# Kernel tuning notes

Measured on AMD Instinct MI355X. Metric: run time of the kernel, lower is better.

## Reference

```python
import jax, jax.numpy as jnp
import numpy as np

N_NODES = 50000
N_EDGES = 800000
D_FEAT = 64
N_CLASSES = 40


def setup_inputs() -> dict:
    key = jax.random.key(0)
    ks = jax.random.split(key, 8)
    x = jax.random.normal(ks[0], (N_NODES, D_FEAT), dtype=jnp.float32)
    edge_index = jax.random.randint(ks[1], (2, N_EDGES), 0, N_NODES, dtype=jnp.int64)
    # GCNConv weights (glorot-ish scale) and post-aggregation biases
    s1 = 1.0 / np.sqrt(D_FEAT)
    W1 = jax.random.normal(ks[2], (D_FEAT, D_FEAT), dtype=jnp.float32) * s1
    b1 = jnp.zeros((D_FEAT,), dtype=jnp.float32)
    W2 = jax.random.normal(ks[3], (D_FEAT, D_FEAT), dtype=jnp.float32) * s1
    b2 = jnp.zeros((D_FEAT,), dtype=jnp.float32)
    W3 = jax.random.normal(ks[4], (D_FEAT, N_CLASSES), dtype=jnp.float32) * s1
    b3 = jnp.zeros((N_CLASSES,), dtype=jnp.float32)
    return {"x": x, "edge_index": edge_index, "W1": W1, "b1": b1,
            "W2": W2, "b2": b2, "W3": W3, "b3": b3}


def _gcn_layer(x, src, dst, norm, W, b, n_nodes):
    # dense transform then normalized neighbor aggregation (PyG GCNConv)
    h = x @ W                                   # [N, out]
    msgs = h[src] * norm[:, None]               # gather over edges [E+N, out]
    agg = jax.ops.segment_sum(msgs, dst, num_segments=n_nodes)
    return agg + b


def reference(x, edge_index, W1, b1, W2, b2, W3, b3):
    n = x.shape[0]
    loops = jnp.arange(n, dtype=edge_index.dtype)
    src = jnp.concatenate([edge_index[0], loops])   # add self-loops
    dst = jnp.concatenate([edge_index[1], loops])
    # symmetric normalization: deg over targets incl. self-loops
    deg = jax.ops.segment_sum(jnp.ones_like(dst, dtype=x.dtype), dst, num_segments=n)
    dinv = jnp.where(deg > 0, jax.lax.rsqrt(deg), 0.0)
    norm = dinv[src] * dinv[dst]                    # [E+N]
    for W, b in ((W1, b1), (W2, b2), (W3, b3)):
        x = jax.nn.relu(_gcn_layer(x, src, dst, norm, W, b, n))
        # dropout treated as identity (deterministic eval reference)
    return jax.nn.log_softmax(x, axis=-1)
```

## Files before the change

kernel.cpp:

```cpp
#include <hip/hip_runtime.h>
#include <math.h>


#define DF 64
#define TB 256
#define NPART 8

__device__ __forceinline__ unsigned short f2bf(float f) {
    union { float f; unsigned u; } c; c.f = f;
    unsigned u = c.u;
    return (unsigned short)((u + 0x7fffu + ((u >> 16) & 1u)) >> 16);
}
__device__ __forceinline__ float bf2f(unsigned short h) {
    union { unsigned u; float f; } c; c.u = ((unsigned)h) << 16;
    return c.f;
}

__global__ void zero_int_kernel(int* __restrict__ p, int n) {
    int i = blockIdx.x * blockDim.x + threadIdx.x;
    if (i < n) p[i] = 0;
}

__global__ void count_deg_part_kernel(const int* __restrict__ dst, int* __restrict__ deg,
                                      int e, int psize) {
    const int p   = blockIdx.x & (NPART - 1);
    const int sl  = blockIdx.x / NPART;
    const int nsl = gridDim.x / NPART;
    const int lo = p * psize, hi = lo + psize;
    for (int i = sl * TB + threadIdx.x; i < e; i += nsl * TB) {
        int d = dst[i];
        if (d >= lo && d < hi) atomicAdd(&deg[d], 1);
    }
}

__global__ void scan_block_kernel(const int* __restrict__ deg, int* __restrict__ ex,
                                  int* __restrict__ bsum, float* __restrict__ dinv, int n) {
    __shared__ int s[TB];
    const int t = threadIdx.x;
    const int i = blockIdx.x * TB + t;
    int v = (i < n) ? deg[i] : 0;
    if (i < n) dinv[i] = rsqrtf((float)(v + 1));
    s[t] = v; __syncthreads();
#pragma unroll
    for (int o = 1; o < TB; o <<= 1) {
        int u = (t >= o) ? s[t - o] : 0;
        __syncthreads();
        s[t] += u;
        __syncthreads();
    }
    if (i < n) ex[i] = s[t] - v;
    if (t == TB - 1) bsum[blockIdx.x] = s[TB - 1];
}

__global__ void scan_sums_kernel(int* __restrict__ bsum, int nb) {
    __shared__ int s[TB];
    const int t = threadIdx.x;
    int v = (t < nb) ? bsum[t] : 0;
    s[t] = v; __syncthreads();
#pragma unroll
    for (int o = 1; o < TB; o <<= 1) {
        int u = (t >= o) ? s[t - o] : 0;
        __syncthreads();
        s[t] += u;
        __syncthreads();
    }
    if (t < nb) bsum[t] = s[t] - v;
}

__global__ void add_offsets_kernel(int* __restrict__ ex, const int* __restrict__ bsum,
                                   int* __restrict__ cursor, int n) {
    int i = blockIdx.x * blockDim.x + threadIdx.x;
    if (i < n) {
        int r = ex[i] + bsum[blockIdx.x];
        ex[i] = r;
        cursor[i] = r;
    }
}

__global__ void fill_csr_part_kernel(const int* __restrict__ src, const int* __restrict__ dst,
                                     int* __restrict__ cursor,
                                     unsigned short* __restrict__ cidx, int e, int psize) {
    const int p   = blockIdx.x & (NPART - 1);
    const int sl  = blockIdx.x / NPART;
    const int nsl = gridDim.x / NPART;
    const int lo = p * psize, hi = lo + psize;
    for (int i = sl * TB + threadIdx.x; i < e; i += nsl * TB) {
        int d = dst[i];
        if (d >= lo && d < hi) {
            int pos = atomicAdd(&cursor[d], 1);
            cidx[pos] = (unsigned short)src[i];
        }
    }
}

template <int NC, typename TIN>
__global__ __launch_bounds__(256) void gemm_kernel(const TIN* __restrict__ X,
                                                   const float* __restrict__ W,
                                                   const float* __restrict__ dinv,
                                                   unsigned short* __restrict__ G, int M) {
    __shared__ float Ws[64 * NC];
    __shared__ float Xs[16][65];
    const int tx = threadIdx.x;
    const int ty = threadIdx.y;
    const int tid = ty * 16 + tx;
    for (int i = tid; i < 64 * NC / 4; i += 256)
        ((float4*)Ws)[i] = ((const float4*)W)[i];
    const int row0 = blockIdx.x * 16;
    {
        int r = tid / 16, c4 = tid % 16;
        bool ok = (row0 + r < M);
        if (sizeof(TIN) == 4) {
            const float* Xf = (const float*)X;
            float4 v = ok ? ((const float4*)(Xf + (size_t)(row0 + r) * 64))[c4]
                          : make_float4(0.f, 0.f, 0.f, 0.f);
            Xs[r][c4 * 4 + 0] = v.x; Xs[r][c4 * 4 + 1] = v.y;
            Xs[r][c4 * 4 + 2] = v.z; Xs[r][c4 * 4 + 3] = v.w;
        } else {
            const unsigned short* Xh = (const unsigned short*)X;
            ushort4 v = ok ? ((const ushort4*)(Xh + (size_t)(row0 + r) * 64))[c4]
                           : make_ushort4(0, 0, 0, 0);
            Xs[r][c4 * 4 + 0] = bf2f(v.x); Xs[r][c4 * 4 + 1] = bf2f(v.y);
            Xs[r][c4 * 4 + 2] = bf2f(v.z); Xs[r][c4 * 4 + 3] = bf2f(v.w);
        }
    }
    __syncthreads();
    const int row = row0 + ty;
    const int c0 = tx * 4;
    if (row < M && c0 < NC) {
        float a0 = 0.f, a1 = 0.f, a2 = 0.f, a3 = 0.f;
#pragma unroll
        for (int k = 0; k < 64; ++k) {
            float xk = Xs[ty][k];
            float4 w = ((const float4*)(Ws + (size_t)k * NC))[tx];
            a0 += xk * w.x; a1 += xk * w.y; a2 += xk * w.z; a3 += xk * w.w;
        }
        float di = dinv[row];
        ushort4 o;
        o.x = f2bf(a0 * di); o.y = f2bf(a1 * di);
        o.z = f2bf(a2 * di); o.w = f2bf(a3 * di);
        *((ushort4*)(G + (size_t)row * NC + c0)) = o;
    }
}

template <int NC, typename TOUT, bool LSM>
__global__ void agg_kernel(const unsigned short* __restrict__ G,
                           const int* __restrict__ rowptr, const int* __restrict__ deg,
                           const unsigned short* __restrict__ cidx,
                           const float* __restrict__ dinv, const float* __restrict__ b,
                           TOUT* __restrict__ Y, int M) {
    const int lane = threadIdx.x & 63;
    const int node = blockIdx.x * 4 + (threadIdx.x >> 6);
    if (node >= M) return;
    const bool act = (lane < NC);
    const int start = rowptr[node];
    const int cnt = deg[node];

    float a0 = act ? bf2f(G[(size_t)node * NC + lane]) : 0.0f;
    float a1 = 0.f, a2 = 0.f, a3 = 0.f;

    for (int base = 0; base < cnt; base += 64) {
        const int nthis = min(64, cnt - base);
        int myidx = (lane < nthis) ? (int)cidx[start + base + lane] : 0;
        int j = 0;
        for (; j + 3 < nthis; j += 4) {
            int s0 = __shfl(myidx, j, 64);
            int s1 = __shfl(myidx, j + 1, 64);
            int s2 = __shfl(myidx, j + 2, 64);
            int s3 = __shfl(myidx, j + 3, 64);
            if (act) {
                a0 += bf2f(G[(size_t)s0 * NC + lane]);
                a1 += bf2f(G[(size_t)s1 * NC + lane]);
                a2 += bf2f(G[(size_t)s2 * NC + lane]);
                a3 += bf2f(G[(size_t)s3 * NC + lane]);
            }
        }
        for (; j < nthis; ++j) {
            int s = __shfl(myidx, j, 64);
            if (act) a1 += bf2f(G[(size_t)s * NC + lane]);
        }
    }
    float v = (a0 + a1 + a2 + a3) * dinv[node] + (act ? b[lane] : 0.0f);
    v = fmaxf(v, 0.0f);

    if (!LSM) {
        if (act) {
            if (sizeof(TOUT) == 2) ((unsigned short*)Y)[(size_t)node * NC + lane] = f2bf(v);
            else                   ((float*)Y)[(size_t)node * NC + lane] = v;
        }
        return;
    }
    float vm = act ? v : -INFINITY;
    float m = vm;
#pragma unroll
    for (int o = 32; o; o >>= 1) m = fmaxf(m, __shfl_xor(m, o, 64));
    float ex = act ? expf(vm - m) : 0.0f;
    float s = ex;
#pragma unroll
    for (int o = 32; o; o >>= 1) s += __shfl_xor(s, o, 64);
    if (act) ((float*)Y)[(size_t)node * NC + lane] = vm - m - logf(s);
}

extern "C" void kernel_launch(void* const* d_in, const int* in_sizes, int n_in,
                              void* d_out, int out_size, void* d_ws, size_t ws_size,
                              hipStream_t stream) {
    const float* x  = (const float*)d_in[0];
    const int*   ei = (const int*)d_in[1];
    const float* W1 = (const float*)d_in[2];
    const float* b1 = (const float*)d_in[3];
    const float* W2 = (const float*)d_in[4];
    const float* b2 = (const float*)d_in[5];
    const float* W3 = (const float*)d_in[6];
    const float* b3 = (const float*)d_in[7];
    float* out = (float*)d_out;

    const int M  = in_sizes[0] / DF;
    const int E  = in_sizes[1] / 2;
    (void)ws_size; (void)n_in; (void)out_size;

    const int* src = ei;
    const int* dst = ei + E;

    const size_t Ma = ((size_t)M + 63) & ~63ull;
    const size_t Ea = ((size_t)E + 63) & ~63ull;

    int* deg    = (int*)d_ws;
    int* rowptr = deg + Ma;
    int* cursor = rowptr + Ma;
    int* bsum   = cursor + Ma;
    unsigned short* cidx = (unsigned short*)(bsum + 256);
    float* dinv = (float*)(cidx + Ea);
    unsigned short* G    = (unsigned short*)(dinv + Ma);
    unsigned short* Bact = G + Ma * DF;

    const int gN = (M + TB - 1) / TB;
    const int nb = gN;
    const int psize = (M + NPART - 1) / NPART;
    const int partGrd = NPART * 96;

    zero_int_kernel<<<gN, TB, 0, stream>>>(deg, M);
    count_deg_part_kernel<<<partGrd, TB, 0, stream>>>(dst, deg, E, psize);
    scan_block_kernel<<<nb, TB, 0, stream>>>(deg, rowptr, bsum, dinv, M);
    scan_sums_kernel<<<1, TB, 0, stream>>>(bsum, nb);
    add_offsets_kernel<<<nb, TB, 0, stream>>>(rowptr, bsum, cursor, M);
    fill_csr_part_kernel<<<partGrd, TB, 0, stream>>>(src, dst, cursor, cidx, E, psize);

    const dim3 gemmBlk(16, 16);
    const int  gemmGrd = (M + 15) / 16;
    const int  aggGrd  = (M + 3) / 4;

    gemm_kernel<64, float><<<gemmGrd, gemmBlk, 0, stream>>>(x, W1, dinv, G, M);
    agg_kernel<64, unsigned short, false><<<aggGrd, TB, 0, stream>>>(G, rowptr, deg, cidx, dinv, b1, Bact, M);
    gemm_kernel<64, unsigned short><<<gemmGrd, gemmBlk, 0, stream>>>(Bact, W2, dinv, G, M);
    agg_kernel<64, unsigned short, false><<<aggGrd, TB, 0, stream>>>(G, rowptr, deg, cidx, dinv, b2, Bact, M);
    gemm_kernel<40, unsigned short><<<gemmGrd, gemmBlk, 0, stream>>>(Bact, W3, dinv, G, M);
    agg_kernel<40, float, true><<<aggGrd, TB, 0, stream>>>(G, rowptr, deg, cidx, dinv, b3, out, M);
}
```

Measured before the change: 224.7 us.

## Vectorize GCN aggregation gathers and fold block-sum scan into offset kernel

The aggregation kernel now splits each 64-lane wavefront into four 16-lane groups. Each group gathers a different neighbor row with 8-byte bf16x4 loads, and the partial sums are reduced across groups with xor shuffles. This gives fewer, wider memory transactions and more independent gathers in flight per wave, in exchange for extra shuffle reductions and idle lanes for the 40-class layer. Separately, the single-block scan of block sums is merged into the add-offsets kernel, where every block recomputes the scan redundantly, which removes one kernel launch.

```diff
diff --git a/kernel.cpp b/kernel.cpp
--- a/kernel.cpp
+++ b/kernel.cpp
@@ -14,6 +14,12 @@
 __device__ __forceinline__ float bf2f(unsigned short h) {
     union { unsigned u; float f; } c; c.u = ((unsigned)h) << 16;
     return c.f;
+}
+__device__ __forceinline__ void acc_bf16x4(uint2 v, float* a) {
+    a[0] += bf2f((unsigned short)(v.x & 0xffffu));
+    a[1] += bf2f((unsigned short)(v.x >> 16));
+    a[2] += bf2f((unsigned short)(v.y & 0xffffu));
+    a[3] += bf2f((unsigned short)(v.y >> 16));
 }
 
 __global__ void zero_int_kernel(int* __restrict__ p, int n) {
@@ -52,7 +58,8 @@
     if (t == TB - 1) bsum[blockIdx.x] = s[TB - 1];
 }
 
-__global__ void scan_sums_kernel(int* __restrict__ bsum, int nb) {
+__global__ void add_offsets_kernel(int* __restrict__ ex, const int* __restrict__ bsum,
+                                   int* __restrict__ cursor, int n, int nb) {
     __shared__ int s[TB];
     const int t = threadIdx.x;
     int v = (t < nb) ? bsum[t] : 0;
@@ -64,14 +71,10 @@
         s[t] += u;
         __syncthreads();
     }
-    if (t < nb) bsum[t] = s[t] - v;
-}
-
-__global__ void add_offsets_kernel(int* __restrict__ ex, const int* __restrict__ bsum,
-                                   int* __restrict__ cursor, int n) {
-    int i = blockIdx.x * blockDim.x + threadIdx.x;
+    const int boff = (blockIdx.x > 0) ? s[blockIdx.x - 1] : 0;
+    const int i = blockIdx.x * TB + t;
     if (i < n) {
-        int r = ex[i] + bsum[blockIdx.x];
+        int r = ex[i] + boff;
         ex[i] = r;
         cursor[i] = r;
     }
@@ -148,56 +151,100 @@
                            const unsigned short* __restrict__ cidx,
                            const float* __restrict__ dinv, const float* __restrict__ b,
                            TOUT* __restrict__ Y, int M) {
+    constexpr int NQ = NC / 4;
     const int lane = threadIdx.x & 63;
     const int node = blockIdx.x * 4 + (threadIdx.x >> 6);
     if (node >= M) return;
-    const bool act = (lane < NC);
+    const int grp = lane >> 4;
+    const int sub = lane & 15;
+    const bool act = (sub < NQ);
     const int start = rowptr[node];
     const int cnt = deg[node];
 
-    float a0 = act ? bf2f(G[(size_t)node * NC + lane]) : 0.0f;
-    float a1 = 0.f, a2 = 0.f, a3 = 0.f;
+    float a[4] = {0.f, 0.f, 0.f, 0.f};
+    float c[4] = {0.f, 0.f, 0.f, 0.f};
 
     for (int base = 0; base < cnt; base += 64) {
         const int nthis = min(64, cnt - base);
         int myidx = (lane < nthis) ? (int)cidx[start + base + lane] : 0;
         int j = 0;
-        for (; j + 3 < nthis; j += 4) {
-            int s0 = __shfl(myidx, j, 64);
-            int s1 = __shfl(myidx, j + 1, 64);
-            int s2 = __shfl(myidx, j + 2, 64);
-            int s3 = __shfl(myidx, j + 3, 64);
+        for (; j + 8 <= nthis; j += 8) {
+            int s0 = __shfl(myidx, j + grp, 64);
+            int s1 = __shfl(myidx, j + 4 + grp, 64);
             if (act) {
-                a0 += bf2f(G[(size_t)s0 * NC + lane]);
-                a1 += bf2f(G[(size_t)s1 * NC + lane]);
-                a2 += bf2f(G[(size_t)s2 * NC + lane]);
-                a3 += bf2f(G[(size_t)s3 * NC + lane]);
+                uint2 v0 = *(const uint2*)(G + (size_t)s0 * NC + sub * 4);
+                uint2 v1 = *(const uint2*)(G + (size_t)s1 * NC + sub * 4);
+                acc_bf16x4(v0, a);
+                acc_bf16x4(v1, c);
             }
         }
-        for (; j < nthis; ++j) {
-            int s = __shfl(myidx, j, 64);
-            if (act) a1 += bf2f(G[(size_t)s * NC + lane]);
-        }
-    }
-    float v = (a0 + a1 + a2 + a3) * dinv[node] + (act ? b[lane] : 0.0f);
-    v = fmaxf(v, 0.0f);
+        if (j + 4 <= nthis) {
+            int s0 = __shfl(myidx, j + grp, 64);
+            if (act) {
+                uint2 v0 = *(const uint2*)(G + (size_t)s0 * NC + sub * 4);
+                acc_bf16x4(v0, a);
+            }
+            j += 4;
+        }
+        const int rem = nthis - j;
+        if (grp < rem) {
+            int s0 = __shfl(myidx, j + grp, 64);
+            if (act) {
+                uint2 v0 = *(const uint2*)(G + (size_t)s0 * NC + sub * 4);
+                acc_bf16x4(v0, c);
+            }
+        }
+    }
+#pragma unroll
+    for (int k = 0; k < 4; ++k) a[k] += c[k];
+#pragma unroll
+    for (int k = 0; k < 4; ++k) {
+        a[k] += __shfl_xor(a[k], 16, 64);
+        a[k] += __shfl_xor(a[k], 32, 64);
+    }
+    float v[4];
+    {
+        float self[4] = {0.f, 0.f, 0.f, 0.f};
+        float4 bb = make_float4(0.f, 0.f, 0.f, 0.f);
+        if (act) {
+            uint2 sv = *(const uint2*)(G + (size_t)node * NC + sub * 4);
+            self[0] = bf2f((unsigned short)(sv.x & 0xffffu));
+            self[1] = bf2f((unsigned short)(sv.x >> 16));
+            self[2] = bf2f((unsigned short)(sv.y & 0xffffu));
+            self[3] = bf2f((unsigned short)(sv.y >> 16));
+            bb = *(const float4*)(b + sub * 4);
+        }
+        const float di = dinv[node];
+        v[0] = fmaxf((a[0] + self[0]) * di + bb.x, 0.f);
+        v[1] = fmaxf((a[1] + self[1]) * di + bb.y, 0.f);
+        v[2] = fmaxf((a[2] + self[2]) * di + bb.z, 0.f);
+        v[3] = fmaxf((a[3] + self[3]) * di + bb.w, 0.f);
+    }
 
     if (!LSM) {
-        if (act) {
-            if (sizeof(TOUT) == 2) ((unsigned short*)Y)[(size_t)node * NC + lane] = f2bf(v);
-            else                   ((float*)Y)[(size_t)node * NC + lane] = v;
+        if (act && grp == 0) {
+            if (sizeof(TOUT) == 2) {
+                ushort4 o;
+                o.x = f2bf(v[0]); o.y = f2bf(v[1]); o.z = f2bf(v[2]); o.w = f2bf(v[3]);
+                *((ushort4*)((unsigned short*)Y + (size_t)node * NC + sub * 4)) = o;
+            } else {
+                *((float4*)((float*)Y + (size_t)node * NC + sub * 4)) =
+                    make_float4(v[0], v[1], v[2], v[3]);
+            }
         }
         return;
     }
-    float vm = act ? v : -INFINITY;
-    float m = vm;
-#pragma unroll
-    for (int o = 32; o; o >>= 1) m = fmaxf(m, __shfl_xor(m, o, 64));
-    float ex = act ? expf(vm - m) : 0.0f;
-    float s = ex;
-#pragma unroll
-    for (int o = 32; o; o >>= 1) s += __shfl_xor(s, o, 64);
-    if (act) ((float*)Y)[(size_t)node * NC + lane] = vm - m - logf(s);
+    float m = act ? fmaxf(fmaxf(v[0], v[1]), fmaxf(v[2], v[3])) : -INFINITY;
+#pragma unroll
+    for (int o = 1; o < 16; o <<= 1) m = fmaxf(m, __shfl_xor(m, o, 64));
+    float es = act ? (expf(v[0] - m) + expf(v[1] - m) + expf(v[2] - m) + expf(v[3] - m)) : 0.f;
+#pragma unroll
+    for (int o = 1; o < 16; o <<= 1) es += __shfl_xor(es, o, 64);
+    const float ls = logf(es);
+    if (act && grp == 0) {
+        *((float4*)((float*)Y + (size_t)node * NC + sub * 4)) =
+            make_float4(v[0] - m - ls, v[1] - m - ls, v[2] - m - ls, v[3] - m - ls);
+    }
 }
 
 extern "C" void kernel_launch(void* const* d_in, const int* in_sizes, int n_in,
@@ -240,8 +287,7 @@
     zero_int_kernel<<<gN, TB, 0, stream>>>(deg, M);
     count_deg_part_kernel<<<partGrd, TB, 0, stream>>>(dst, deg, E, psize);
     scan_block_kernel<<<nb, TB, 0, stream>>>(deg, rowptr, bsum, dinv, M);
-    scan_sums_kernel<<<1, TB, 0, stream>>>(bsum, nb);
-    add_offsets_kernel<<<nb, TB, 0, stream>>>(rowptr, bsum, cursor, M);
+    add_offsets_kernel<<<nb, TB, 0, stream>>>(rowptr, bsum, cursor, M, nb);
     fill_csr_part_kernel<<<partGrd, TB, 0, stream>>>(src, dst, cursor, cidx, E, psize);
 
     const dim3 gemmBlk(16, 16);
```

Result: faster. 214.9 us (-4.4%).
